# Kernel optimization log

Measured on AMD Instinct MI355X. Metric: run time of the kernel, lower is better.

## Reference

```python
import jax, jax.numpy as jnp
import numpy as np

B, N_HEADS, DIM, Z, X = 128, 12, 768, 7, 14


def _rpe_index(z, x):
    """2D concatenated self-attention relative positional encoding index.
    Tokens = z*z template tokens followed by x*x search tokens. Two token
    pairs share a bias index iff they have the same (dh, dw, region_i, region_j).
    """
    zh, zw = np.meshgrid(np.arange(z), np.arange(z), indexing='ij')
    xh, xw = np.meshgrid(np.arange(x), np.arange(x), indexing='ij')
    h = np.concatenate([zh.ravel(), xh.ravel()])
    w = np.concatenate([zw.ravel(), xw.ravel()])
    region = np.concatenate([np.zeros(z * z, np.int64), np.ones(x * x, np.int64)])
    dh = h[:, None] - h[None, :]
    dw = w[:, None] - w[None, :]
    rb = np.broadcast_to(region[:, None], dh.shape)
    rc = np.broadcast_to(region[None, :], dh.shape)
    key = np.stack([dh, dw, rb, rc], axis=-1).reshape(-1, 4)
    _, inv = np.unique(key, axis=0, return_inverse=True)
    return inv.reshape(dh.shape)  # (N, N) int


def setup_inputs() -> dict:
    key = jax.random.key(0)
    ks = jax.random.split(key, 4)
    N = Z * Z + X * X  # 245
    idx = _rpe_index(Z, X)
    n_bias = int(idx.max()) + 1
    return {
        "x": jax.random.normal(ks[0], (B, N, DIM), jnp.float32),
        "qkv_w": jax.random.normal(ks[1], (3 * DIM, DIM), jnp.float32) * 0.02,
        "proj_w": jax.random.normal(ks[2], (DIM, DIM), jnp.float32) * 0.02,
        "proj_b": jnp.zeros((DIM,), jnp.float32),
        "bias_table": jax.random.normal(ks[3], (N_HEADS, n_bias), jnp.float32) * 0.02,
        "rel_index": jnp.asarray(idx, jnp.int32),
    }


def reference(x, qkv_w, proj_w, proj_b, bias_table, rel_index):
    Bq, N, C = x.shape
    H = N_HEADS
    Dh = C // H
    scale = Dh ** -0.5
    # qkv projection (no bias): (B, N, 3, H, Dh)
    qkv = (x @ qkv_w.T).reshape(Bq, N, 3, H, Dh)
    q = jnp.moveaxis(qkv[:, :, 0], 2, 1)  # (B, H, N, Dh)
    k = jnp.moveaxis(qkv[:, :, 1], 2, 1)
    v = jnp.moveaxis(qkv[:, :, 2], 2, 1)
    attn = jnp.einsum('bhnd,bhmd->bhnm', q, k) * scale  # (B, H, N, N)
    # relative position bias gather: (H, N, N) broadcast over batch
    attn = attn + bias_table[:, rel_index][None]
    attn = jax.nn.softmax(attn, axis=-1)
    out = jnp.einsum('bhnm,bhmd->bhnd', attn, v)  # (B, H, N, Dh)
    out = jnp.moveaxis(out, 1, 2).reshape(Bq, N, C)
    return out @ proj_w.T + proj_b
```

## Files before the change

kernel.cpp:

```cpp
#include <hip/hip_runtime.h>
#include <hip/hip_bf16.h>
#include <stdint.h>

#define BATCH 128
#define NTOK 245
#define HEADS 12
#define DHEAD 64
#define CDIM 768
#define KT 24
#define SUBT 512

typedef __attribute__((ext_vector_type(8))) short short8;
typedef __attribute__((ext_vector_type(4))) float f32x4;

__device__ __forceinline__ float bf2f(uint32_t hbits) {
    union { uint32_t u; float f; } v; v.u = hbits << 16; return v.f;
}
__device__ __forceinline__ uint32_t f2bf(float f) {
    union { float f; uint32_t u; } v; v.f = f;
    return (v.u + 0x7fffu + ((v.u >> 16) & 1u)) >> 16;
}
__device__ __forceinline__ ushort2 pk2bf(float x, float y) {
    union { __hip_bfloat162 h; ushort2 u; } c;
    c.h = __float22bfloat162_rn(make_float2(x, y));
    return c.u;
}
__device__ __forceinline__ size_t tiled_addr(int m, int k) {
    return (((size_t)(m >> 4) * KT + (k >> 5)) * 64 + ((k >> 3) & 3) * 16 + (m & 15)) * 8
           + (k & 7);
}
__device__ __forceinline__ void gl_lds16(const uint16_t* g, ushort* lds) {
    __builtin_amdgcn_global_load_lds(
        (const __attribute__((address_space(1))) void*)g,
        (__attribute__((address_space(3))) void*)lds,
        16, 0, 0);
}

__global__ __launch_bounds__(256)
void cvt_tile_bf16(const float* __restrict__ src, uint16_t* __restrict__ dst, int n8)
{
    int i = blockIdx.x * 256 + threadIdx.x;
    const int stride = gridDim.x * 256;
    for (; i < n8; i += stride) {
        const int sl = i & 63;
        const int tile = i >> 6;
        const int rt = tile / KT, kt = tile - rt * KT;
        const size_t soff = (size_t)(rt * 16 + (sl & 15)) * CDIM + kt * 32 + (sl >> 4) * 8;
        float4 a = *(const float4*)(src + soff);
        float4 b = *(const float4*)(src + soff + 4);
        ushort2 p0 = pk2bf(a.x, a.y), p1 = pk2bf(a.z, a.w);
        ushort2 p2 = pk2bf(b.x, b.y), p3 = pk2bf(b.z, b.w);
        uint4 o;
        o.x = (uint32_t)p0.x | ((uint32_t)p0.y << 16);
        o.y = (uint32_t)p1.x | ((uint32_t)p1.y << 16);
        o.z = (uint32_t)p2.x | ((uint32_t)p2.y << 16);
        o.w = (uint32_t)p3.x | ((uint32_t)p3.y << 16);
        *(uint4*)(dst + (size_t)i * 8) = o;
    }
}

__global__ __launch_bounds__(256)
void bias_pre(const float* __restrict__ bias_table, const int* __restrict__ rel,
              int n_bias, uint16_t* __restrict__ bias_t)
{
    const int h = blockIdx.x, j = blockIdx.y, q = threadIdx.x;
    float v = -30000.f;
    if (j < NTOK && q < NTOK) v = bias_table[(size_t)h * n_bias + rel[q * NTOK + j]];
    bias_t[((size_t)h * 256 + j) * 256 + q] = (uint16_t)f2bf(v);
}

#define GEMM_LOOP                                                                \
    gl_lds16(gA0, &Af[0][w  ][0][0]);                                            \
    gl_lds16(gA1, &Af[0][w+4][0][0]);                                            \
    gl_lds16(gB0, &Bf[0][w  ][0][0]);                                            \
    gl_lds16(gB1, &Bf[0][w+4][0][0]);                                            \
    gl_lds16(gA0 + SUBT, &Af[1][w  ][0][0]);                                     \
    gl_lds16(gA1 + SUBT, &Af[1][w+4][0][0]);                                     \
    gl_lds16(gB0 + SUBT, &Bf[1][w  ][0][0]);                                     \
    gl_lds16(gB1 + SUBT, &Bf[1][w+4][0][0]);                                     \
    int cur = 0, nxt = 2;                                                        \
    _Pragma("unroll 1")                                                          \
    for (int t = 0; t < KT; ++t) {                                               \
        if (t == KT - 1) { asm volatile("s_waitcnt vmcnt(0) lgkmcnt(0)" ::: "memory"); } \
        else             { asm volatile("s_waitcnt vmcnt(4) lgkmcnt(0)" ::: "memory"); } \
        __builtin_amdgcn_s_barrier();                                            \
        if (t + 2 < KT) {                                                        \
            const int ko = (t + 2) * SUBT;                                       \
            gl_lds16(gA0 + ko, &Af[nxt][w  ][0][0]);                             \
            gl_lds16(gA1 + ko, &Af[nxt][w+4][0][0]);                             \
            gl_lds16(gB0 + ko, &Bf[nxt][w  ][0][0]);                             \
            gl_lds16(gB1 + ko, &Bf[nxt][w+4][0][0]);                             \
        }                                                                        \
        short8 af[4], bf[4];                                                     \
        _Pragma("unroll")                                                        \
        for (int m = 0; m < 4; ++m)                                              \
            af[m] = *(const short8*)&Af[cur][wr*4 + m][l][0];                    \
        _Pragma("unroll")                                                        \
        for (int n = 0; n < 4; ++n)                                              \
            bf[n] = *(const short8*)&Bf[cur][wc*4 + n][l][0];                    \
        _Pragma("unroll")                                                        \
        for (int m = 0; m < 4; ++m)                                              \
            _Pragma("unroll")                                                    \
            for (int n = 0; n < 4; ++n)                                          \
                acc[m][n] = __builtin_amdgcn_mfma_f32_16x16x32_bf16(bf[n], af[m], acc[m][n], 0, 0, 0); \
        cur = (cur == 2) ? 0 : cur + 1;                                          \
        nxt = (nxt == 2) ? 0 : nxt + 1;                                          \
    }

__global__ __launch_bounds__(256)
void qkv_gemm_mfma(const uint16_t* __restrict__ xb, const uint16_t* __restrict__ wq,
                   uint16_t* __restrict__ qkv)
{
    __shared__ ushort Af[3][8][64][8];
    __shared__ ushort Bf[3][8][64][8];
    const int t = threadIdx.x;
    const int w = t >> 6, l = t & 63;
    const int wr = w >> 1, wc = w & 1;
    const int lm = l & 15, lk = l >> 4;

    const int bid = blockIdx.x;
    const int xcd = bid & 7;
    const int wg = (xcd < 2 ? xcd * 552 : 1104 + (xcd - 2) * 551) + (bid >> 3);
    const int mtile = wg / 18, ctile = wg - mtile * 18;
    const int m0 = mtile * 128, c0 = ctile * 128;

    const uint16_t* gA0 = xb + ((size_t)(mtile*8 + w    ) * KT * 64 + l) * 8;
    const uint16_t* gA1 = xb + ((size_t)(mtile*8 + w + 4) * KT * 64 + l) * 8;
    const uint16_t* gB0 = wq + ((size_t)(ctile*8 + w    ) * KT * 64 + l) * 8;
    const uint16_t* gB1 = wq + ((size_t)(ctile*8 + w + 4) * KT * 64 + l) * 8;

    f32x4 acc[4][4];
    #pragma unroll
    for (int m = 0; m < 4; ++m)
        #pragma unroll
        for (int n = 0; n < 4; ++n) acc[m][n] = (f32x4){0.f,0.f,0.f,0.f};

    GEMM_LOOP

    int sArr[4], hArr[4], dArr[4];
    #pragma unroll
    for (int n = 0; n < 4; ++n) {
        int c = c0 + wc*64 + n*16 + lk*4;
        int s = c / CDIM; int rem = c - s * CDIM;
        sArr[n] = s; hArr[n] = rem >> 6; dArr[n] = rem & 63;
    }
    #pragma unroll
    for (int m = 0; m < 4; ++m) {
        int gm  = m0 + wr*64 + m*16 + lm;
        int b   = gm / NTOK;
        int tok = gm - b * NTOK;
        #pragma unroll
        for (int n = 0; n < 4; ++n) {
            ushort2 u0 = pk2bf(acc[m][n][0], acc[m][n][1]);
            ushort2 u1 = pk2bf(acc[m][n][2], acc[m][n][3]);
            uint2 pk;
            pk.x = (uint32_t)u0.x | ((uint32_t)u0.y << 16);
            pk.y = (uint32_t)u1.x | ((uint32_t)u1.y << 16);
            size_t addr = ((((size_t)b*3 + sArr[n])*HEADS + hArr[n])*NTOK + tok)*DHEAD + dArr[n];
            *(uint2*)(qkv + addr) = pk;
        }
    }
}

__global__ __launch_bounds__(512)
void attn_mfma(const uint16_t* __restrict__ qkv, const uint16_t* __restrict__ bias_t,
               uint16_t* __restrict__ o_t)
{
    __shared__ ushort Ks[256][72];
    __shared__ ushort Vt[64][264];
    __shared__ ushort Ps[8][16][72];
    const int bh = blockIdx.x;
    const int b = bh / HEADS, h = bh % HEADS;
    const int t = threadIdx.x;
    const int w = t >> 6, l = t & 63;
    const int lm = l & 15, lk = l >> 4;
    const int wq0 = w * 32;

    const uint16_t* qbase = qkv + (((size_t)b*3 + 0)*HEADS + h) * (NTOK*DHEAD);
    const uint16_t* kbase = qkv + (((size_t)b*3 + 1)*HEADS + h) * (NTOK*DHEAD);
    const uint16_t* vbase = qkv + (((size_t)b*3 + 2)*HEADS + h) * (NTOK*DHEAD);
    const uint16_t* btab  = bias_t + (size_t)h * 256 * 256;

    {
        const int col = (t & 7) * 8;
        #pragma unroll
        for (int p = 0; p < 4; ++p) {
            int row = p * 64 + (t >> 3);
            uint4 val = make_uint4(0u,0u,0u,0u);
            if (row < NTOK) val = *(const uint4*)(kbase + (size_t)row * DHEAD + col);
            *(uint4*)&Ks[row][col] = val;
        }
    }
    {
        const int j  = t >> 1;
        const int dh = (t & 1) * 32;
        uint4 r0 = make_uint4(0,0,0,0), r1 = r0, r2 = r0, r3 = r0;
        if (j < NTOK) {
            const uint16_t* src = vbase + (size_t)j * DHEAD + dh;
            r0 = *(const uint4*)(src);
            r1 = *(const uint4*)(src + 8);
            r2 = *(const uint4*)(src + 16);
            r3 = *(const uint4*)(src + 24);
        }
        union { uint4 v[4]; ushort s[32]; } u;
        u.v[0] = r0; u.v[1] = r1; u.v[2] = r2; u.v[3] = r3;
        #pragma unroll
        for (int i = 0; i < 32; ++i)
            Vt[dh + i][j] = u.s[i];
    }

    short8 qf[2][2];
    #pragma unroll
    for (int m = 0; m < 2; ++m) {
        int qrow = wq0 + m*16 + lm; if (qrow > NTOK-1) qrow = NTOK-1;
        #pragma unroll
        for (int k2 = 0; k2 < 2; ++k2)
            qf[m][k2] = *(const short8*)(qbase + (size_t)qrow * DHEAD + k2*32 + lk*8);
    }

    f32x4 acc_o[2][4];
    float lsum[2][4];
    #pragma unroll
    for (int m = 0; m < 2; ++m) {
        #pragma unroll
        for (int n = 0; n < 4; ++n) acc_o[m][n] = (f32x4){0.f,0.f,0.f,0.f};
        #pragma unroll
        for (int r = 0; r < 4; ++r) lsum[m][r] = 0.f;
    }

    __syncthreads();

    for (int jb = 0; jb < 4; ++jb) {
        short8 kf[4][2], vf[4][2];
        #pragma unroll
        for (int n = 0; n < 4; ++n)
            #pragma unroll
            for (int k2 = 0; k2 < 2; ++k2) {
                kf[n][k2] = *(const short8*)&Ks[jb*64 + n*16 + lm][k2*32 + lk*8];
                vf[n][k2] = *(const short8*)&Vt[n*16 + lm][jb*64 + k2*32 + lk*8];
            }

        #pragma unroll
        for (int m = 0; m < 2; ++m) {
            f32x4 sv[4];
            #pragma unroll
            for (int n = 0; n < 4; ++n) {
                f32x4 z = (f32x4){0.f,0.f,0.f,0.f};
                sv[n] = __builtin_amdgcn_mfma_f32_16x16x32_bf16(qf[m][0], kf[n][0], z, 0, 0, 0);
                sv[n] = __builtin_amdgcn_mfma_f32_16x16x32_bf16(qf[m][1], kf[n][1], sv[n], 0, 0, 0);
            }
            #pragma unroll
            for (int n = 0; n < 4; ++n) {
                uint2 bb = *(const uint2*)(btab + (size_t)(jb*64 + n*16 + lm) * 256 + wq0 + m*16 + lk*4);
                float s0 = fmaf(sv[n][0], 0.125f, bf2f(bb.x & 0xffffu));
                float s1 = fmaf(sv[n][1], 0.125f, bf2f(bb.x >> 16));
                float s2 = fmaf(sv[n][2], 0.125f, bf2f(bb.y & 0xffffu));
                float s3 = fmaf(sv[n][3], 0.125f, bf2f(bb.y >> 16));
                sv[n][0] = __expf(fminf(s0, 30.f));
                sv[n][1] = __expf(fminf(s1, 30.f));
                sv[n][2] = __expf(fminf(s2, 30.f));
                sv[n][3] = __expf(fminf(s3, 30.f));
            }
            #pragma unroll
            for (int n = 0; n < 4; ++n)
                #pragma unroll
                for (int r = 0; r < 4; ++r) {
                    ushort u = (ushort)f2bf(sv[n][r]);
                    lsum[m][r] += bf2f(u);
                    Ps[w][lk*4 + r][n*16 + lm] = u;
                }
            short8 pf[2];
            #pragma unroll
            for (int k2 = 0; k2 < 2; ++k2)
                pf[k2] = *(const short8*)&Ps[w][lm][k2*32 + lk*8];
            #pragma unroll
            for (int n = 0; n < 4; ++n) {
                acc_o[m][n] = __builtin_amdgcn_mfma_f32_16x16x32_bf16(pf[0], vf[n][0], acc_o[m][n], 0, 0, 0);
                acc_o[m][n] = __builtin_amdgcn_mfma_f32_16x16x32_bf16(pf[1], vf[n][1], acc_o[m][n], 0, 0, 0);
            }
        }
    }

    #pragma unroll
    for (int m = 0; m < 2; ++m) {
        float inv[4];
        #pragma unroll
        for (int r = 0; r < 4; ++r) {
            float s = lsum[m][r];
            s += __shfl_xor(s, 1);
            s += __shfl_xor(s, 2);
            s += __shfl_xor(s, 4);
            s += __shfl_xor(s, 8);
            inv[r] = 1.f / s;
        }
        #pragma unroll
        for (int r = 0; r < 4; ++r) {
            int q = wq0 + m*16 + lk*4 + r;
            if (q < NTOK) {
                int gm = b * NTOK + q;
                #pragma unroll
                for (int n = 0; n < 4; ++n) {
                    int k = h * DHEAD + n*16 + lm;
                    o_t[tiled_addr(gm, k)] = (uint16_t)f2bf(acc_o[m][n][r] * inv[r]);
                }
            }
        }
    }
}

__global__ __launch_bounds__(256)
void proj_gemm_mfma(const uint16_t* __restrict__ ot, const uint16_t* __restrict__ wp,
                    const float* __restrict__ bias, float* __restrict__ out)
{
    __shared__ ushort Af[3][8][64][8];
    __shared__ ushort Bf[3][8][64][8];
    const int t = threadIdx.x;
    const int w = t >> 6, l = t & 63;
    const int wr = w >> 1, wc = w & 1;
    const int lm = l & 15, lk = l >> 4;

    const int bid = blockIdx.x;
    const int xcd = bid & 7;
    const int wg = (xcd < 6 ? xcd * 184 : 1104 + (xcd - 6) * 183) + (bid >> 3);
    const int mtile = wg / 6, ctile = wg - mtile * 6;
    const int m0 = mtile * 128, c0 = ctile * 128;

    const uint16_t* gA0 = ot + ((size_t)(mtile*8 + w    ) * KT * 64 + l) * 8;
    const uint16_t* gA1 = ot + ((size_t)(mtile*8 + w + 4) * KT * 64 + l) * 8;
    const uint16_t* gB0 = wp + ((size_t)(ctile*8 + w    ) * KT * 64 + l) * 8;
    const uint16_t* gB1 = wp + ((size_t)(ctile*8 + w + 4) * KT * 64 + l) * 8;

    f32x4 acc[4][4];
    #pragma unroll
    for (int m = 0; m < 4; ++m)
        #pragma unroll
        for (int n = 0; n < 4; ++n) acc[m][n] = (f32x4){0.f,0.f,0.f,0.f};

    GEMM_LOOP

    float4 bsv[4]; int cArr[4];
    #pragma unroll
    for (int n = 0; n < 4; ++n) {
        cArr[n] = c0 + wc*64 + n*16 + lk*4;
        bsv[n]  = *(const float4*)(bias + cArr[n]);
    }
    #pragma unroll
    for (int m = 0; m < 4; ++m) {
        int gm = m0 + wr*64 + m*16 + lm;
        #pragma unroll
        for (int n = 0; n < 4; ++n) {
            float4 r;
            r.x = acc[m][n][0] + bsv[n].x;
            r.y = acc[m][n][1] + bsv[n].y;
            r.z = acc[m][n][2] + bsv[n].z;
            r.w = acc[m][n][3] + bsv[n].w;
            *(float4*)(out + (size_t)gm * CDIM + cArr[n]) = r;
        }
    }
}

extern "C" void kernel_launch(void* const* d_in, const int* in_sizes, int n_in,
                              void* d_out, int out_size, void* d_ws, size_t ws_size,
                              hipStream_t stream)
{
    (void)n_in; (void)out_size;
    const float* x          = (const float*)d_in[0];
    const float* qkv_w      = (const float*)d_in[1];
    const float* proj_w     = (const float*)d_in[2];
    const float* proj_b     = (const float*)d_in[3];
    const float* bias_table = (const float*)d_in[4];
    const int*   rel        = (const int*)d_in[5];
    const int n_bias = in_sizes[4] / HEADS;

    const size_t qkv_elems = (size_t)BATCH * 3 * HEADS * NTOK * DHEAD;
    const size_t o_elems   = (size_t)BATCH * HEADS * NTOK * DHEAD;
    const size_t bt_elems  = (size_t)HEADS * 256 * 256;
    const size_t wq_elems  = (size_t)3 * CDIM * CDIM;
    const size_t wp_elems  = (size_t)CDIM * CDIM;

    uint16_t* qkv_ws = (uint16_t*)d_ws;
    uint16_t* o_ws   = qkv_ws + qkv_elems;
    uint16_t* bt_ws  = o_ws + o_elems;
    uint16_t* wq_ws  = bt_ws + bt_elems;
    uint16_t* wp_ws  = wq_ws + wq_elems;
    const size_t need = (qkv_elems + o_elems + bt_elems + wq_elems + wp_elems) * sizeof(uint16_t);
    if (ws_size < need) return;

    uint16_t* xb = o_ws;

    cvt_tile_bf16<<<2048, 256, 0, stream>>>(x, xb, (int)(o_elems / 8));
    cvt_tile_bf16<<<864, 256, 0, stream>>>(qkv_w, wq_ws, (int)(wq_elems / 8));
    cvt_tile_bf16<<<288, 256, 0, stream>>>(proj_w, wp_ws, (int)(wp_elems / 8));

    bias_pre<<<dim3(HEADS, 256), 256, 0, stream>>>(bias_table, rel, n_bias, bt_ws);

    qkv_gemm_mfma<<<4410, 256, 0, stream>>>(xb, wq_ws, qkv_ws);

    attn_mfma<<<dim3(BATCH * HEADS), 512, 0, stream>>>(qkv_ws, bt_ws, o_ws);

    proj_gemm_mfma<<<1470, 256, 0, stream>>>(o_ws, wp_ws, proj_b, (float*)d_out);
}
```

Measured before the change: 322.1 us.

## Merge conversion launches, use exp2 softmax, add MFMA priority hints

Folds the three fp32-to-bf16 conversion launches into one grid-stride kernel to cut launch overhead and tail effects. Folds log2(e) into the bias table and the QK scale so the softmax uses exp2f instead of __expf, with the clamps adjusted to match. Wraps the MFMA sections of the attention kernel in s_setprio hints and uses the hardware bf16 pack for P. Each change is small, and the merged conversion adds a branch per element to pick the source tensor.

New measurement: 321.6 us (median of 2 runs). No clear change (-0.1%).

```diff
diff --git a/kernel.cpp b/kernel.cpp
--- a/kernel.cpp
+++ b/kernel.cpp
@@ -1,6 +1,7 @@
 #include <hip/hip_runtime.h>
 #include <hip/hip_bf16.h>
 #include <stdint.h>
+#include <math.h>
 
 #define BATCH 128
 #define NTOK 245
@@ -9,6 +10,8 @@
 #define CDIM 768
 #define KT 24
 #define SUBT 512
+#define SCL 0.18033688f
+#define PCLAMP 43.3f
 
 typedef __attribute__((ext_vector_type(8))) short short8;
 typedef __attribute__((ext_vector_type(4))) float f32x4;
@@ -36,14 +39,24 @@
         16, 0, 0);
 }
 
+#define N8_X  3010560
+#define N8_WQ  221184
+#define N8_WP   73728
 __global__ __launch_bounds__(256)
-void cvt_tile_bf16(const float* __restrict__ src, uint16_t* __restrict__ dst, int n8)
+void cvt_all(const float* __restrict__ x, const float* __restrict__ wq,
+             const float* __restrict__ wp, uint16_t* __restrict__ xd,
+             uint16_t* __restrict__ wqd, uint16_t* __restrict__ wpd)
 {
     int i = blockIdx.x * 256 + threadIdx.x;
     const int stride = gridDim.x * 256;
-    for (; i < n8; i += stride) {
-        const int sl = i & 63;
-        const int tile = i >> 6;
+    const int total = N8_X + N8_WQ + N8_WP;
+    for (; i < total; i += stride) {
+        const float* src; uint16_t* dst; int j;
+        if (i < N8_X)              { src = x;  dst = xd;  j = i; }
+        else if (i < N8_X + N8_WQ) { src = wq; dst = wqd; j = i - N8_X; }
+        else                       { src = wp; dst = wpd; j = i - N8_X - N8_WQ; }
+        const int sl = j & 63;
+        const int tile = j >> 6;
         const int rt = tile / KT, kt = tile - rt * KT;
         const size_t soff = (size_t)(rt * 16 + (sl & 15)) * CDIM + kt * 32 + (sl >> 4) * 8;
         float4 a = *(const float4*)(src + soff);
@@ -55,7 +68,7 @@
         o.y = (uint32_t)p1.x | ((uint32_t)p1.y << 16);
         o.z = (uint32_t)p2.x | ((uint32_t)p2.y << 16);
         o.w = (uint32_t)p3.x | ((uint32_t)p3.y << 16);
-        *(uint4*)(dst + (size_t)i * 8) = o;
+        *(uint4*)(dst + (size_t)j * 8) = o;
     }
 }
 
@@ -64,8 +77,9 @@
               int n_bias, uint16_t* __restrict__ bias_t)
 {
     const int h = blockIdx.x, j = blockIdx.y, q = threadIdx.x;
-    float v = -30000.f;
-    if (j < NTOK && q < NTOK) v = bias_table[(size_t)h * n_bias + rel[q * NTOK + j]];
+    float v = -43281.f;
+    if (j < NTOK && q < NTOK)
+        v = bias_table[(size_t)h * n_bias + rel[q * NTOK + j]] * 1.44269504f;
     bias_t[((size_t)h * 256 + j) * 256 + q] = (uint16_t)f2bf(v);
 }
 
@@ -243,29 +257,31 @@
         #pragma unroll
         for (int m = 0; m < 2; ++m) {
             f32x4 sv[4];
+            __builtin_amdgcn_s_setprio(1);
             #pragma unroll
             for (int n = 0; n < 4; ++n) {
                 f32x4 z = (f32x4){0.f,0.f,0.f,0.f};
                 sv[n] = __builtin_amdgcn_mfma_f32_16x16x32_bf16(qf[m][0], kf[n][0], z, 0, 0, 0);
                 sv[n] = __builtin_amdgcn_mfma_f32_16x16x32_bf16(qf[m][1], kf[n][1], sv[n], 0, 0, 0);
             }
+            __builtin_amdgcn_s_setprio(0);
             #pragma unroll
             for (int n = 0; n < 4; ++n) {
                 uint2 bb = *(const uint2*)(btab + (size_t)(jb*64 + n*16 + lm) * 256 + wq0 + m*16 + lk*4);
-                float s0 = fmaf(sv[n][0], 0.125f, bf2f(bb.x & 0xffffu));
-                float s1 = fmaf(sv[n][1], 0.125f, bf2f(bb.x >> 16));
-                float s2 = fmaf(sv[n][2], 0.125f, bf2f(bb.y & 0xffffu));
-                float s3 = fmaf(sv[n][3], 0.125f, bf2f(bb.y >> 16));
-                sv[n][0] = __expf(fminf(s0, 30.f));
-                sv[n][1] = __expf(fminf(s1, 30.f));
-                sv[n][2] = __expf(fminf(s2, 30.f));
-                sv[n][3] = __expf(fminf(s3, 30.f));
+                float s0 = fmaf(sv[n][0], SCL, bf2f(bb.x & 0xffffu));
+                float s1 = fmaf(sv[n][1], SCL, bf2f(bb.x >> 16));
+                float s2 = fmaf(sv[n][2], SCL, bf2f(bb.y & 0xffffu));
+                float s3 = fmaf(sv[n][3], SCL, bf2f(bb.y >> 16));
+                sv[n][0] = exp2f(fminf(s0, PCLAMP));
+                sv[n][1] = exp2f(fminf(s1, PCLAMP));
+                sv[n][2] = exp2f(fminf(s2, PCLAMP));
+                sv[n][3] = exp2f(fminf(s3, PCLAMP));
             }
             #pragma unroll
             for (int n = 0; n < 4; ++n)
                 #pragma unroll
                 for (int r = 0; r < 4; ++r) {
-                    ushort u = (ushort)f2bf(sv[n][r]);
+                    ushort u = pk2bf(sv[n][r], sv[n][r]).x;
                     lsum[m][r] += bf2f(u);
                     Ps[w][lk*4 + r][n*16 + lm] = u;
                 }
@@ -273,11 +289,13 @@
             #pragma unroll
             for (int k2 = 0; k2 < 2; ++k2)
                 pf[k2] = *(const short8*)&Ps[w][lm][k2*32 + lk*8];
+            __builtin_amdgcn_s_setprio(1);
             #pragma unroll
             for (int n = 0; n < 4; ++n) {
                 acc_o[m][n] = __builtin_amdgcn_mfma_f32_16x16x32_bf16(pf[0], vf[n][0], acc_o[m][n], 0, 0, 0);
                 acc_o[m][n] = __builtin_amdgcn_mfma_f32_16x16x32_bf16(pf[1], vf[n][1], acc_o[m][n], 0, 0, 0);
             }
+            __builtin_amdgcn_s_setprio(0);
         }
     }
 
@@ -388,9 +406,7 @@
 
     uint16_t* xb = o_ws;
 
-    cvt_tile_bf16<<<2048, 256, 0, stream>>>(x, xb, (int)(o_elems / 8));
-    cvt_tile_bf16<<<864, 256, 0, stream>>>(qkv_w, wq_ws, (int)(wq_elems / 8));
-    cvt_tile_bf16<<<288, 256, 0, stream>>>(proj_w, wp_ws, (int)(wp_elems / 8));
+    cvt_all<<<2048, 256, 0, stream>>>(x, qkv_w, proj_w, xb, wq_ws, wp_ws);
 
     bias_pre<<<dim3(HEADS, 256), 256, 0, stream>>>(bias_table, rel, n_bias, bt_ws);
 
```
